# Kernel tuning notes

Hardware: AMD Instinct MI355X
Metric: run time of the kernel (lower is better)

Reference implementation:

```python
import jax, jax.numpy as jnp
import numpy as np

PI = float(np.pi)
N_DIST, N_THETA = 4, 8   # projection_dict
MAX_DIST = 0.2           # self.max_dist (estimated from nh distances in __init__)


def _distance_angle(lon1, lat1, lon2, lat2):
    # great-circle distance + bearing ('polar' base of get_distance_angle)
    dlon = lon2 - lon1
    cos_d = jnp.sin(lat1) * jnp.sin(lat2) + jnp.cos(lat1) * jnp.cos(lat2) * jnp.cos(dlon)
    d = jnp.arccos(jnp.clip(cos_d, -1.0 + 1e-7, 1.0 - 1e-7))
    phi = jnp.arctan2(jnp.sin(dlon) * jnp.cos(lat2),
                      jnp.cos(lat1) * jnp.sin(lat2) - jnp.sin(lat1) * jnp.cos(lat2) * jnp.cos(dlon))
    return d, phi


def _forward(x, coordinates, sigma_d, kappa_vm, local_indices, adjc):
    # x: [B,N,E]; adjc: [Ncells,NH]; coordinates: [2,Ncells]; local_indices: [B,N]
    sigma_d = jnp.reshape(sigma_d, ())
    kappa_vm = jnp.reshape(kappa_vm, ())
    indices_nh = adjc[local_indices]                              # [B,N,NH] (get_nh_indices)
    # gather_nh_data (sample offsets are zero: sampled_level == global_level, sample==0)
    x_nh = jax.vmap(lambda xb, ib: xb[ib])(x, indices_nh)         # [B,N,NH,E]
    coords_nh = coordinates[:, indices_nh]                        # [2,B,N,NH]
    # get_relative_positions(coords_nh[:,:,:,0], coords_nh, polar=True):
    # coords1 -> [2,B,N,1,1], coords2 -> [2,B,N,1,NH]  => dists/phis [B,N,1,NH]
    lon_c = coords_nh[0, :, :, 0][..., None, None]                # [B,N,1,1]
    lat_c = coords_nh[1, :, :, 0][..., None, None]
    lon_nh = coords_nh[0][:, :, None, :]                          # [B,N,1,NH]
    lat_nh = coords_nh[1][:, :, None, :]
    dists, phis = _distance_angle(lon_c, lat_c, lon_nh, lat_nh)   # [B,N,1,NH]
    thetas_proj = jnp.linspace(-PI, PI, N_THETA + 1)[:-1]         # [T]
    dists_proj = jnp.linspace(0.0, MAX_DIST, N_DIST)              # [D]
    # von_mises: [D?,T,1] - [B,N,1,1,NH] broadcast -> we keep factored forms
    vm = jnp.exp(kappa_vm * jnp.cos(thetas_proj[None, :, None] - phis[..., None, :]))        # [B,N,1,T,NH]
    nd = jnp.exp(-0.5 * ((dists_proj[:, None, None] - dists[..., None, :]) / sigma_d) ** 2)  # [B,N,D,1,NH]
    w = vm * nd                                                   # [B,N,D,T,NH]
    w = w / (w.sum(axis=-1, keepdims=True) + 1e-10)
    # proj_data: weighted sum over neighborhood -> [B,N,D,T,E]
    return jnp.einsum('bndtk,bnke->bndte', w, x_nh)


def setup_inputs() -> dict:
    key = jax.random.key(0)
    k1, k2, k3 = jax.random.split(key, 3)
    B, N, NH, E = 1, 65536, 7, 16
    x = jax.random.normal(k1, (B, N, E), dtype=jnp.float32)
    # lon/lat in a small local patch (radians) so neighbor distances are O(MAX_DIST)
    coordinates = jax.random.uniform(k2, (2, N), dtype=jnp.float32) * 0.2
    adjc = jax.random.randint(k3, (N, NH), 0, N, dtype=jnp.int32)
    local_indices = jnp.arange(N, dtype=jnp.int32)[None, :]       # [B,N]
    sigma_d = jnp.full((1,), 0.05, dtype=jnp.float32)
    kappa_vm = jnp.full((1,), 2.0, dtype=jnp.float32)
    return {"x": x, "coordinates": coordinates, "sigma_d": sigma_d,
            "kappa_vm": kappa_vm, "local_indices": local_indices, "adjc": adjc}


def reference(x, coordinates, sigma_d, kappa_vm, local_indices, adjc):
    return _forward(x, coordinates, sigma_d, kappa_vm, local_indices, adjc)
```

## Files before the change

kernel.cpp:

```cpp
#include <hip/hip_runtime.h>
#include <math.h>

constexpr int NH     = 7;
constexpr int NDIST  = 4;
constexpr int NTHETA = 8;
constexpr int EDIM   = 16;
constexpr int NPB    = 8;
constexpr int BLOCK  = 256;

__global__ __launch_bounds__(BLOCK) void grid_layer_kernel(
    const float* __restrict__ x,
    const float* __restrict__ coords,
    const float* __restrict__ sigma_p,
    const float* __restrict__ kappa_p,
    const int*   __restrict__ lidx,
    const int*   __restrict__ adjc,
    float*       __restrict__ out,
    int N)
{
    __shared__ float2 geom[NPB][NH];
    __shared__ float4 xs[NPB][NH][EDIM / 4];

    const int tid = threadIdx.x;
    const int n0  = blockIdx.x * NPB;

    const float sigma   = sigma_p[0];
    const float kappa   = kappa_p[0];
    const float inv_s   = 1.0f / sigma;

    if (tid < NPB * NH * 4) {
        const int p  = tid >> 2;
        const int q  = tid & 3;
        const int nl = p / NH;
        const int k  = p - nl * NH;
        const int n  = n0 + nl;
        if (n < N) {
            const int idx = adjc[(size_t)lidx[n] * NH + k];
            xs[nl][k][q] = ((const float4*)(x + (size_t)idx * EDIM))[q];
        }
    }

    if (tid < NPB * NH) {
        const int nl = tid / NH;
        const int k  = tid - nl * NH;
        const int n  = n0 + nl;
        if (n < N) {
            const int li   = lidx[n];
            const int idx0 = adjc[(size_t)li * NH];
            const int idxk = adjc[(size_t)li * NH + k];
            const float lon1 = coords[idx0], lat1 = coords[N + idx0];
            const float lon2 = coords[idxk], lat2 = coords[N + idxk];
            const float dlon = lon2 - lon1;
            const float sl1 = sinf(lat1), cl1 = cosf(lat1);
            const float sl2 = sinf(lat2), cl2 = cosf(lat2);
            const float sdl = sinf(dlon), cdl = cosf(dlon);
            float cos_d = sl1 * sl2 + cl1 * cl2 * cdl;
            cos_d = fminf(fmaxf(cos_d, -1.0f + 1e-7f), 1.0f - 1e-7f);
            const float dist = acosf(cos_d);
            const float phi  = atan2f(sdl * cl2, cl1 * sl2 - sl1 * cl2 * cdl);
            geom[nl][k] = make_float2(dist, phi);
        }
    }
    __syncthreads();

    const int nl = tid >> 5;
    const int j  = tid & 31;
    const int t  = j >> 2;
    const int e4 = j & 3;
    const int n  = n0 + nl;
    if (n >= N) return;

    const float theta = -3.14159265358979f + (float)t * 0.78539816339745f;

    float w[NDIST][NH];
    #pragma unroll
    for (int k = 0; k < NH; ++k) {
        const float2 g   = geom[nl][k];
        const float  ang = kappa * cosf(theta - g.y);
        #pragma unroll
        for (int d = 0; d < NDIST; ++d) {
            const float dp = 0.066666667f * (float)d;
            const float z  = (dp - g.x) * inv_s;
            w[d][k] = expf(ang - 0.5f * z * z);
        }
    }
    #pragma unroll
    for (int d = 0; d < NDIST; ++d) {
        float s = 0.0f;
        #pragma unroll
        for (int k = 0; k < NH; ++k) s += w[d][k];
        const float inv = 1.0f / (s + 1e-10f);
        #pragma unroll
        for (int k = 0; k < NH; ++k) w[d][k] *= inv;
    }

    float4 acc[NDIST];
    #pragma unroll
    for (int d = 0; d < NDIST; ++d) acc[d] = make_float4(0.f, 0.f, 0.f, 0.f);
    #pragma unroll
    for (int k = 0; k < NH; ++k) {
        const float4 xv = xs[nl][k][e4];
        #pragma unroll
        for (int d = 0; d < NDIST; ++d) {
            acc[d].x += w[d][k] * xv.x;
            acc[d].y += w[d][k] * xv.y;
            acc[d].z += w[d][k] * xv.z;
            acc[d].w += w[d][k] * xv.w;
        }
    }

    float4* outp = (float4*)(out + (size_t)n * (NDIST * NTHETA * EDIM));
    #pragma unroll
    for (int d = 0; d < NDIST; ++d) {
        outp[d * (NTHETA * EDIM / 4) + t * (EDIM / 4) + e4] = acc[d];
    }
}

extern "C" void kernel_launch(void* const* d_in, const int* in_sizes, int n_in,
                              void* d_out, int out_size, void* d_ws, size_t ws_size,
                              hipStream_t stream) {
    const float* x      = (const float*)d_in[0];
    const float* coords = (const float*)d_in[1];
    const float* sigma  = (const float*)d_in[2];
    const float* kappa  = (const float*)d_in[3];
    const int*   lidx   = (const int*)d_in[4];
    const int*   adjc   = (const int*)d_in[5];
    float*       out    = (float*)d_out;

    const int N = in_sizes[4];
    const int grid = (N + NPB - 1) / NPB;
    hipLaunchKernelGGL(grid_layer_kernel, dim3(grid), dim3(BLOCK), 0, stream,
                       x, coords, sigma, kappa, lidx, adjc, out, N);
}
```

Measured before the change: 174.0 us.

## Factor von Mises and normal weights into shared memory and defer normalization

Splits the weight exp(kappa*cos + gaussian) into a product of separately precomputed von Mises (per theta, neighbor) and normal (per dist, neighbor) factors stored in shared memory. This avoids recomputing 28 expf and 7 cosf per thread, which were redundant across the four e4 lanes. Normalization is deferred to the end, scaling the accumulators by the reciprocal of the weight sum. The cost is an extra barrier, extra shared memory, and a small numeric difference from factoring the exponential.

Result: faster. 162.8 us (-6.4%).

```diff
diff --git a/kernel.cpp b/kernel.cpp
--- a/kernel.cpp
+++ b/kernel.cpp
@@ -20,13 +20,15 @@
 {
     __shared__ float2 geom[NPB][NH];
     __shared__ float4 xs[NPB][NH][EDIM / 4];
+    __shared__ float  vm_s[NPB][NTHETA][NH];
+    __shared__ float  nd_s[NPB][NDIST][NH];
 
     const int tid = threadIdx.x;
     const int n0  = blockIdx.x * NPB;
 
-    const float sigma   = sigma_p[0];
-    const float kappa   = kappa_p[0];
-    const float inv_s   = 1.0f / sigma;
+    const float sigma = sigma_p[0];
+    const float kappa = kappa_p[0];
+    const float inv_s = 1.0f / sigma;
 
     if (tid < NPB * NH * 4) {
         const int p  = tid >> 2;
@@ -59,6 +61,30 @@
             const float dist = acosf(cos_d);
             const float phi  = atan2f(sdl * cl2, cl1 * sl2 - sl1 * cl2 * cdl);
             geom[nl][k] = make_float2(dist, phi);
+            #pragma unroll
+            for (int d = 0; d < NDIST; ++d) {
+                const float dp = 0.066666667f * (float)d;
+                const float z  = (dp - dist) * inv_s;
+                nd_s[nl][d][k] = expf(-0.5f * z * z);
+            }
+        }
+    }
+    __syncthreads();
+
+    if (tid < NPB * NH * 4) {
+        const int nl  = tid / (NH * 4);
+        const int r   = tid - nl * (NH * 4);
+        const int k   = r >> 2;
+        const int th2 = r & 3;
+        const int n   = n0 + nl;
+        if (n < N) {
+            const float phi = geom[nl][k].y;
+            #pragma unroll
+            for (int i = 0; i < 2; ++i) {
+                const int t = th2 * 2 + i;
+                const float theta = -3.14159265358979f + (float)t * 0.78539816339745f;
+                vm_s[nl][t][k] = expf(kappa * cosf(theta - phi));
+            }
         }
     }
     __syncthreads();
@@ -70,48 +96,31 @@
     const int n  = n0 + nl;
     if (n >= N) return;
 
-    const float theta = -3.14159265358979f + (float)t * 0.78539816339745f;
-
-    float w[NDIST][NH];
-    #pragma unroll
-    for (int k = 0; k < NH; ++k) {
-        const float2 g   = geom[nl][k];
-        const float  ang = kappa * cosf(theta - g.y);
-        #pragma unroll
-        for (int d = 0; d < NDIST; ++d) {
-            const float dp = 0.066666667f * (float)d;
-            const float z  = (dp - g.x) * inv_s;
-            w[d][k] = expf(ang - 0.5f * z * z);
-        }
-    }
-    #pragma unroll
-    for (int d = 0; d < NDIST; ++d) {
-        float s = 0.0f;
-        #pragma unroll
-        for (int k = 0; k < NH; ++k) s += w[d][k];
-        const float inv = 1.0f / (s + 1e-10f);
-        #pragma unroll
-        for (int k = 0; k < NH; ++k) w[d][k] *= inv;
-    }
-
+    float  s[NDIST]   = {0.f, 0.f, 0.f, 0.f};
     float4 acc[NDIST];
     #pragma unroll
     for (int d = 0; d < NDIST; ++d) acc[d] = make_float4(0.f, 0.f, 0.f, 0.f);
+
     #pragma unroll
     for (int k = 0; k < NH; ++k) {
-        const float4 xv = xs[nl][k][e4];
+        const float  vmk = vm_s[nl][t][k];
+        const float4 xv  = xs[nl][k][e4];
         #pragma unroll
         for (int d = 0; d < NDIST; ++d) {
-            acc[d].x += w[d][k] * xv.x;
-            acc[d].y += w[d][k] * xv.y;
-            acc[d].z += w[d][k] * xv.z;
-            acc[d].w += w[d][k] * xv.w;
+            const float w = vmk * nd_s[nl][d][k];
+            s[d] += w;
+            acc[d].x += w * xv.x;
+            acc[d].y += w * xv.y;
+            acc[d].z += w * xv.z;
+            acc[d].w += w * xv.w;
         }
     }
 
     float4* outp = (float4*)(out + (size_t)n * (NDIST * NTHETA * EDIM));
     #pragma unroll
     for (int d = 0; d < NDIST; ++d) {
+        const float inv = 1.0f / (s[d] + 1e-10f);
+        acc[d].x *= inv; acc[d].y *= inv; acc[d].z *= inv; acc[d].w *= inv;
         outp[d * (NTHETA * EDIM / 4) + t * (EDIM / 4) + e4] = acc[d];
     }
 }
```
